# Kernel optimization log

Measured on AMD Instinct MI355X. Metric: run time of the kernel, lower is better.

Reference implementation:

```python
import jax, jax.numpy as jnp
import numpy as np
from jax import lax

# ---- static config (from BasePllay_2 / AdTopoLayer(out_features=50, T=25, m0=0.2, lims=[[224,0],[0,224]], K_max=2, p=0)) ----
H = W = 28
G = H * W
T = 25
K_MAX = 2
M0 = 0.2
OUT_FEATURES = 50
B = 32
TSEQ = jnp.linspace(0.0, 100.0, T)  # fixed landscape sample grid (covers DTM value range)

# static grid geometry from lims=[[224,0],[0,224]]
_xs = np.linspace(224.0, 0.0, H)
_ys = np.linspace(0.0, 224.0, W)
_pts = np.stack(np.meshgrid(_xs, _ys, indexing="ij"), -1).reshape(G, 2)
_d = np.sqrt(((_pts[:, None] - _pts[None]) ** 2).sum(-1))
_sidx = np.argsort(_d, axis=-1)
SDIST = jnp.asarray(np.take_along_axis(_d, _sidx, -1), jnp.float32)  # [G,G] sorted distances per grid point
SIDX = jnp.asarray(_sidx.astype(np.int32))                            # [G,G] static distance-sort order

# 4-connectivity neighbor table for the cubical (pixel) grid, -1 = invalid
_ii = np.arange(G).reshape(H, W)
_nb = np.full((H, W, 4), -1, np.int32)
_nb[1:, :, 0] = _ii[:-1, :]
_nb[:-1, :, 1] = _ii[1:, :]
_nb[:, 1:, 2] = _ii[:, :-1]
_nb[:, :-1, 3] = _ii[:, 1:]
NBR = jnp.asarray(_nb.reshape(G, 4))


def dtm(w):
    """Weighted distance-to-measure (r=2) on the fixed grid. w: [B,G] nonneg -> [B,G]."""
    sw = w[:, SIDX]                               # [B,G,G] weights in distance order
    cw = jnp.cumsum(sw, -1)
    d2 = SDIST ** 2
    cwd = jnp.cumsum(sw * d2[None], -1)
    bound = M0 * w.sum(-1)                        # [B]
    k = jnp.argmax(cw >= bound[:, None, None], -1)  # [B,G] first index reaching mass bound
    km1 = jnp.maximum(k - 1, 0)
    take = lambda a, i: jnp.take_along_axis(a, i[..., None], -1)[..., 0]
    has_prev = k > 0
    cw_p = jnp.where(has_prev, take(cw, km1), 0.0)
    cwd_p = jnp.where(has_prev, take(cwd, km1), 0.0)
    dk2 = d2[jnp.arange(G)[None, :], k]           # [B,G]
    val = (cwd_p + (bound[:, None] - cw_p) * dk2) / bound[:, None]
    return jnp.sqrt(jnp.maximum(val, 0.0))


def pd0(vals):
    """0-dim sublevel-set persistence of vals on the pixel grid (union-find, elder rule).
    Returns (births[G], deaths[G]); non-merging pixels yield zero-persistence pairs,
    essential components die at the max filtration value."""
    order = jnp.argsort(vals).astype(jnp.int32)
    rank = jnp.zeros(G, jnp.int32).at[order].set(jnp.arange(G, dtype=jnp.int32))

    def find(parent, i):
        return lax.while_loop(lambda j: parent[j] != j, lambda j: parent[j], i)

    def step(s, carry):
        parent, death = carry
        p = order[s]
        best = p
        for t in range(4):  # unrolled over the 4 grid neighbors (static)
            q = NBR[p, t]
            ok = (q >= 0) & (rank[jnp.maximum(q, 0)] < s)  # neighbor already inserted
            r = find(parent, jnp.where(ok, q, p))
            merge = ok & (r != best)
            r_old = rank[r] < rank[best]
            older = jnp.where(r_old, r, best)
            younger = jnp.where(r_old, best, r)
            widx = jnp.where(merge, younger, G)   # slot G is a dummy
            parent = parent.at[widx].set(older)
            death = death.at[widx].set(p)         # younger component dies at pixel p
            best = jnp.where(merge, older, best)
        return parent, death

    parent0 = jnp.arange(G + 1, dtype=jnp.int32)
    death0 = jnp.full(G + 1, -1, jnp.int32)
    _, death = lax.fori_loop(0, G, step, (parent0, death0))
    d = death[:G]
    deaths = jnp.where(d >= 0, vals[jnp.maximum(d, 0)], vals.max())
    return vals, deaths


def landscape(births, deaths):
    """K_MAX persistence landscapes sampled at TSEQ. [B,G] -> [B, K_MAX*T]."""
    tb = TSEQ[None, :, None] - births[:, None, :]   # [B,T,G]
    td = deaths[:, None, :] - TSEQ[None, :, None]
    tent = jnp.maximum(jnp.minimum(tb, td), 0.0)
    topk = lax.top_k(tent, K_MAX)[0]                # [B,T,K]
    return jnp.transpose(topk, (0, 2, 1)).reshape(births.shape[0], K_MAX * T)


def _forward(x, w_land, b_land, w_fc, b_fc):
    w = x.reshape(x.shape[0], -1)          # nn.Flatten: pixel intensities as measure weights
    v = dtm(w)                             # [B,G]
    births, deaths = jax.vmap(pd0)(v)
    feats = landscape(births, deaths)      # [B, 50]
    xt = feats @ w_land.T + b_land         # AdTopoLayer output [B, out_features]
    signal = jnp.abs(lax.stop_gradient(xt)).sum(0)   # torch: x.detach().abs().sum(0)
    out = jnp.maximum(xt, 0.0) @ w_fc.T + b_fc       # fc(relu(x))
    return out, signal

_forward_jit = jax.jit(_forward)


def setup_inputs() -> dict:
    key = jax.random.key(0)
    k = jax.random.split(key, 4)
    x = jax.random.uniform(k[0], (B, 1, H, W), jnp.float32)  # image-like nonneg weights
    w_land = jax.random.normal(k[1], (OUT_FEATURES, K_MAX * T), jnp.float32) * 0.1
    b_land = jnp.zeros((OUT_FEATURES,), jnp.float32)
    w_fc = jax.random.normal(k[2], (10, OUT_FEATURES), jnp.float32) * 0.1
    b_fc = jnp.zeros((10,), jnp.float32)
    return {"x": x, "w_land": w_land, "b_land": b_land, "w_fc": w_fc, "b_fc": b_fc}


def reference(x, w_land, b_land, w_fc, b_fc):
    return _forward_jit(x, w_land, b_land, w_fc, b_fc)
```

## Files before the change

### kernel.cpp

```cpp
#include <hip/hip_runtime.h>
#include <math.h>

#define H28 28
#define G784 784
#define BATCH 32
#define NOFF 3025
#define NOFFP 3072
#define NKEY 1459
#define TPTS 25
#define KMAX 2
#define NFEAT 50
#define OUTF 50
#define NCLS 10

#define NBX 16
#define BT 512
#define BT2 512
#define HS 2048
#define EMAX 1024

struct OffPair { unsigned ij; float d2; };
struct OffTab  { OffPair e[NOFFP]; };

constexpr double csqrt(double x) {
  double r = x * 0.5 + 1.0;
  for (int i = 0; i < 20; i++) r = 0.5 * (r + x / r);
  return r;
}

constexpr OffTab make_offtab() {
  OffTab t{};
  int start[NKEY] = {};
  for (int i = 0; i < NOFF; i++) {
    int di = i / 55 - 27, dj = i % 55 - 27;
    start[di * di + dj * dj]++;
  }
  int run = 0;
  for (int k = 0; k < NKEY; k++) { int h = start[k]; start[k] = run; run += h; }
  for (int i = 0; i < NOFF; i++) {
    int di = i / 55 - 27, dj = i % 55 - 27;
    int key = di * di + dj * dj;
    int pos = start[key]++;
    float sd = (key == 0) ? 0.0f : (float)(csqrt((double)key) * (224.0 / 27.0));
    t.e[pos].ij = ((unsigned)(di & 0xffff)) | (((unsigned)(dj & 0xffff)) << 16);
    t.e[pos].d2 = sd * sd;
  }
  for (int i = NOFF; i < NOFFP; i++) { t.e[i].ij = 0x00640064u; t.e[i].d2 = 0.f; }
  return t;
}

__device__ constexpr OffTab OFFTAB = make_offtab();

__device__ __forceinline__ float wave_iscan_f32(float x) {
  int t;
  t = __builtin_amdgcn_update_dpp(0, __float_as_int(x), 0x111, 0xf, 0xf, true);
  x += __int_as_float(t);
  t = __builtin_amdgcn_update_dpp(0, __float_as_int(x), 0x112, 0xf, 0xf, true);
  x += __int_as_float(t);
  t = __builtin_amdgcn_update_dpp(0, __float_as_int(x), 0x114, 0xf, 0xf, true);
  x += __int_as_float(t);
  t = __builtin_amdgcn_update_dpp(0, __float_as_int(x), 0x118, 0xf, 0xf, true);
  x += __int_as_float(t);
  t = __builtin_amdgcn_update_dpp(0, __float_as_int(x), 0x142, 0xa, 0xf, true);
  x += __int_as_float(t);
  t = __builtin_amdgcn_update_dpp(0, __float_as_int(x), 0x143, 0xc, 0xf, true);
  x += __int_as_float(t);
  return x;
}

__global__ __launch_bounds__(BT) void dtm_kernel(const float* __restrict__ x,
                                                 float* __restrict__ v,
                                                 int* __restrict__ done_ctr) {
  __shared__ float w_s[G784];
  __shared__ float red[BT];

  const int tid = threadIdx.x;
  const int b   = blockIdx.x;
  const int bx  = blockIdx.y;

  if (b == 0 && bx == 0 && tid == 0) *done_ctr = 0;

  float ps = 0.f;
  for (int i = tid; i < G784; i += BT) {
    float wv = x[b * G784 + i];
    w_s[i] = wv;
    ps += wv;
  }
  red[tid] = ps;
  __syncthreads();
  for (int off = BT / 2; off > 0; off >>= 1) {
    if (tid < off) red[tid] += red[tid + off];
    __syncthreads();
  }
  const float bound = 0.2f * red[0];

  const int wave = tid >> 6;
  const int lane = tid & 63;
  const int slot = bx * 8 + wave;

  for (int g = slot; g < G784; g += NBX * 8) {
    const int i1 = g / H28, j1 = g % H28;
    float cw = 0.f, cwd = 0.f;
    float cwp = 0.f, cwdp = 0.f, dk2 = 0.f;
    bool crossed = false;
    int o = lane;
    unsigned ij = OFFTAB.e[o].ij;
    float d2v   = OFFTAB.e[o].d2;
    for (int base = 0; base < NOFFP && !crossed; base += 64) {
      int onext = o + 64;
      if (onext >= NOFFP) onext = o;
      const unsigned ij_n = OFFTAB.e[onext].ij;
      const float    d2_n = OFFTAB.e[onext].d2;
      const int di = (short)(ij & 0xffffu);
      const int dj = (short)(ij >> 16);
      const int i2 = i1 + di, j2 = j1 + dj;
      const bool inb = ((unsigned)i2 < (unsigned)H28) & ((unsigned)j2 < (unsigned)H28);
      const float wv = inb ? w_s[i2 * H28 + j2] : 0.f;
      const float wd = wv * d2v;
      const float psw = wave_iscan_f32(wv);
      const float psd = wave_iscan_f32(wd);
      const unsigned long long mask = __ballot(cw + psw >= bound);
      if (mask) {
        const int f = __ffsll((unsigned long long)mask) - 1;
        const float psw_f = __shfl(psw, f);
        const float w_f   = __shfl(wv, f);
        const float psd_f = __shfl(psd, f);
        const float wd_f  = __shfl(wd, f);
        dk2  = __shfl(d2v, f);
        cwp  = cw + (psw_f - w_f);
        cwdp = cwd + (psd_f - wd_f);
        crossed = true;
      } else {
        cw  += __int_as_float(__builtin_amdgcn_readlane(__float_as_int(psw), 63));
        cwd += __int_as_float(__builtin_amdgcn_readlane(__float_as_int(psd), 63));
      }
      ij = ij_n; d2v = d2_n; o = onext;
    }
    const float val = (cwdp + (bound - cwp) * dk2) / bound;
    if (lane == 0) v[b * G784 + g] = sqrtf(fmaxf(val, 0.f));
  }
}

__device__ __forceinline__ unsigned long long pix_key(const float* val_s, int p) {
  return (((unsigned long long)__float_as_uint(val_s[p])) << 10) | (unsigned)p;
}

__global__ __launch_bounds__(BT2) void pd0_kernel(const float* __restrict__ v,
                                                  float* __restrict__ feats,
                                                  int* __restrict__ done_ctr,
                                                  const float* __restrict__ w_land,
                                                  const float* __restrict__ b_land,
                                                  const float* __restrict__ w_fc,
                                                  const float* __restrict__ b_fc,
                                                  float* __restrict__ out) {
  __shared__ float val_s[G784];
  __shared__ int   ptr_s[G784];
  __shared__ int   parent[G784];
  __shared__ unsigned rank_s[G784];
  __shared__ unsigned claims[G784];
  __shared__ float deathv[G784];
  __shared__ int   mlist[G784];
  __shared__ unsigned long long oldkey[G784];
  __shared__ unsigned htag[HS];
  __shared__ unsigned long long hval[HS];
  __shared__ unsigned long long edges[EMAX];
  __shared__ float redf[BT2];
  __shared__ int   mcnt_sh, ecnt_sh, last_sh;
  __shared__ float vmax_sh;
  __shared__ float f_s[BATCH * NFEAT];
  __shared__ float xt_s[BATCH * OUTF];

  const int tid = threadIdx.x;
  const int b   = blockIdx.x;
  if (tid == 0) { mcnt_sh = 0; ecnt_sh = 0; }

  for (int i = tid; i < HS; i += BT2) { htag[i] = 0u; hval[i] = ~0ULL; }

  float pm = -1e30f;
  for (int i = tid; i < G784; i += BT2) {
    float xv = v[b * G784 + i];
    val_s[i] = xv;
    pm = fmaxf(pm, xv);
    rank_s[i] = 0u;
    claims[i] = 0xFFFFFFFFu;
  }
  redf[tid] = pm;
  __syncthreads();
  for (int off = BT2 / 2; off > 0; off >>= 1) {
    if (tid < off) redf[tid] = fmaxf(redf[tid], redf[tid + off]);
    __syncthreads();
  }
  if (tid == 0) vmax_sh = redf[0];
  __syncthreads();
  const float vmax = vmax_sh;

  for (int p = tid; p < G784; p += BT2) {
    unsigned long long kp = pix_key(val_s, p);
    int i = p / H28, j = p % H28;
    int nbs[4];
    nbs[0] = (i > 0)       ? p - H28 : -1;
    nbs[1] = (i < H28 - 1) ? p + H28 : -1;
    nbs[2] = (j > 0)       ? p - 1   : -1;
    nbs[3] = (j < H28 - 1) ? p + 1   : -1;
    int best = p;
    unsigned long long bk = kp;
    for (int t = 0; t < 4; t++) {
      int q = nbs[t];
      if (q >= 0) {
        unsigned long long kq = pix_key(val_s, q);
        if (kq < bk) { bk = kq; best = q; }
      }
    }
    ptr_s[p]  = best;
    parent[p] = p;
    deathv[p] = vmax;
    if (best == p) {
      oldkey[p] = kp;
      int mi = atomicAdd(&mcnt_sh, 1);
      mlist[mi] = p;
    }
  }
  __syncthreads();

  for (int r = 0; r < 10; r++) {
    for (int p = tid; p < G784; p += BT2) ptr_s[p] = ptr_s[ptr_s[p]];
    __syncthreads();
  }

  for (int p = tid; p < G784; p += BT2) {
    unsigned long long kp = pix_key(val_s, p);
    int i = p / H28, j = p % H28;
    int nbs[4];
    nbs[0] = (i > 0)       ? p - H28 : -1;
    nbs[1] = (i < H28 - 1) ? p + H28 : -1;
    nbs[2] = (j > 0)       ? p - 1   : -1;
    nbs[3] = (j < H28 - 1) ? p + 1   : -1;
    int bp = ptr_s[p];
    for (int t = 0; t < 4; t++) {
      int q = nbs[t];
      if (q >= 0) {
        unsigned long long kq = pix_key(val_s, q);
        int bq = ptr_s[q];
        if (kq < kp && bq != bp) {
          unsigned long long key =
              (((unsigned long long)__float_as_uint(val_s[p])) << 32) |
              (((unsigned long long)(unsigned)p) << 22) |
              (((unsigned long long)(unsigned)t) << 20) |
              (((unsigned long long)(unsigned)bp) << 10) |
              ((unsigned long long)(unsigned)bq);
          unsigned lo = (bp < bq) ? (unsigned)bp : (unsigned)bq;
          unsigned hi = (bp < bq) ? (unsigned)bq : (unsigned)bp;
          unsigned pairid = (lo << 10) | hi;
          unsigned idx = (pairid * 2654435761u) >> 21;
          for (;;) {
            unsigned t0 = atomicCAS(&htag[idx], 0u, pairid + 1u);
            if (t0 == 0u || t0 == pairid + 1u) { atomicMin(&hval[idx], key); break; }
            idx = (idx + 1) & (HS - 1);
          }
        }
      }
    }
  }
  __syncthreads();

  for (int i = tid; i < HS; i += BT2) {
    if (htag[i]) {
      int e = atomicAdd(&ecnt_sh, 1);
      if (e < EMAX) edges[e] = hval[i];
    }
  }
  __syncthreads();
  const int ne   = (ecnt_sh < EMAX) ? ecnt_sh : EMAX;
  const int mcnt = mcnt_sh;
  const int wave = tid >> 6;
  const int lane = tid & 63;

  if (wave == 0) {
    if (ne > 1) {
      int n2 = 1;
      while (n2 < ne) n2 <<= 1;
      for (int i = ne + lane; i < n2; i += 64) edges[i] = ~0ULL;
      __threadfence_block();
      for (int kk = 2; kk <= n2; kk <<= 1) {
        for (int jj = kk >> 1; jj > 0; jj >>= 1) {
          for (int i = lane; i < n2; i += 64) {
            int ixj = i ^ jj;
            if (ixj > i) {
              unsigned long long a = edges[i], c = edges[ixj];
              bool up = ((i & kk) == 0);
              if ((a > c) == up) { edges[i] = c; edges[ixj] = a; }
            }
          }
          __threadfence_block();
        }
      }
    }

    int merged = 0;
    const int target = mcnt - 1;
    for (int base = 0; base < ne && merged < target; base += 64) {
      const int idx = base + lane;
      bool unresolved = (idx < ne);
      const unsigned long long e = unresolved ? edges[idx] : 0ULL;
      const int A  = (int)((e >> 10) & 1023u);
      const int Bq = (int)(e & 1023u);
      const float ev = __uint_as_float((unsigned)(e >> 32));
      for (;;) {
        int rA = A, rB = Bq;
        if (unresolved) {
          int xx = A;
          for (;;) { int p1 = parent[xx]; if (p1 == xx) break;
                     int p2 = parent[p1]; parent[xx] = p2; xx = p2; }
          rA = xx;
          xx = Bq;
          for (;;) { int p1 = parent[xx]; if (p1 == xx) break;
                     int p2 = parent[p1]; parent[xx] = p2; xx = p2; }
          rB = xx;
        }
        bool crossing = unresolved && (rA != rB);
        if (unresolved && !crossing) unresolved = false;
        if (__ballot(crossing) == 0ULL) break;
        if (crossing) {
          atomicMin(&claims[rA], (unsigned)lane);
          atomicMin(&claims[rB], (unsigned)lane);
        }
        __threadfence_block();
        bool win = crossing && claims[rA] == (unsigned)lane
                            && claims[rB] == (unsigned)lane;
        __threadfence_block();
        if (crossing) { claims[rA] = 0xFFFFFFFFu; claims[rB] = 0xFFFFFFFFu; }
        if (win) {
          unsigned long long ka = oldkey[rA], kb = oldkey[rB];
          unsigned ra_ = rank_s[rA], rb_ = rank_s[rB];
          int big   = (ra_ > rb_) ? rA : ((rb_ > ra_) ? rB : ((rA < rB) ? rA : rB));
          int small = (big == rA) ? rB : rA;
          parent[small] = big;
          if (ra_ == rb_) rank_s[big] = ra_ + 1u;
          unsigned long long okmin = (ka < kb) ? ka : kb;
          unsigned long long okmax = (ka < kb) ? kb : ka;
          oldkey[big] = okmin;
          int dying = (int)(okmax & 1023u);
          deathv[dying] = ev;
          unresolved = false;
        }
        __threadfence_block();
        merged += (int)__popcll(__ballot(win));
        if (merged >= target) break;
      }
    }
    __threadfence_block();

    if (lane < TPTS) {
      float ti = (float)((double)lane * (100.0 / 24.0));
      float t1 = 0.f, t2 = 0.f;
      for (int ii = 0; ii < mcnt; ii++) {
        int m = mlist[ii];
        float tent = fminf(ti - val_s[m], deathv[m] - ti);
        tent = fmaxf(tent, 0.f);
        if (tent > t1)      { t2 = t1; t1 = tent; }
        else if (tent > t2) { t2 = tent; }
      }
      feats[b * NFEAT + lane]        = t1;
      feats[b * NFEAT + TPTS + lane] = t2;
    }
  }

  __threadfence();
  __syncthreads();
  if (tid == 0) last_sh = (atomicAdd(done_ctr, 1) == BATCH - 1) ? 1 : 0;
  __syncthreads();
  if (!last_sh) return;
  __threadfence();

  for (int i = tid; i < BATCH * NFEAT; i += BT2) f_s[i] = feats[i];
  __syncthreads();
  for (int idx = tid; idx < BATCH * OUTF; idx += BT2) {
    int bb = idx / OUTF, ff = idx % OUTF;
    float acc = b_land[ff];
    const float* wr = w_land + ff * NFEAT;
    const float* fr = f_s + bb * NFEAT;
    for (int j = 0; j < NFEAT; j++) acc += fr[j] * wr[j];
    xt_s[idx] = acc;
  }
  __syncthreads();
  if (tid < OUTF) {
    float s = 0.f;
    for (int bb = 0; bb < BATCH; bb++) s += fabsf(xt_s[bb * OUTF + tid]);
    out[BATCH * NCLS + tid] = s;
  }
  for (int idx = tid; idx < BATCH * NCLS; idx += BT2) {
    int bb = idx / NCLS, cc = idx % NCLS;
    float acc = b_fc[cc];
    const float* wr = w_fc + cc * OUTF;
    const float* xr = xt_s + bb * OUTF;
    for (int ff = 0; ff < OUTF; ff++) acc += fmaxf(xr[ff], 0.f) * wr[ff];
    out[bb * NCLS + cc] = acc;
  }
}

extern "C" void kernel_launch(void* const* d_in, const int* in_sizes, int n_in,
                              void* d_out, int out_size, void* d_ws, size_t ws_size,
                              hipStream_t stream) {
  (void)in_sizes; (void)n_in; (void)out_size; (void)ws_size;
  const float* x      = (const float*)d_in[0];
  const float* w_land = (const float*)d_in[1];
  const float* b_land = (const float*)d_in[2];
  const float* w_fc   = (const float*)d_in[3];
  const float* b_fc   = (const float*)d_in[4];
  float* out   = (float*)d_out;
  float* v     = (float*)d_ws;
  float* feats = v + BATCH * G784;
  int*   done  = (int*)(feats + BATCH * NFEAT);

  dim3 g1(BATCH, NBX);
  dtm_kernel<<<g1, BT, 0, stream>>>(x, v, done);
  pd0_kernel<<<BATCH, BT2, 0, stream>>>(v, feats, done,
                                        w_land, b_land, w_fc, b_fc, out);
}
```

Before: 100.5 us.

## Shrink persistence kernel to one wave, replace bitonic sort with rank sort

```diff
diff --git a/kernel.cpp b/kernel.cpp
--- a/kernel.cpp
+++ b/kernel.cpp
@@ -13,11 +13,12 @@
 #define OUTF 50
 #define NCLS 10
 
-#define NBX 16
+#define NBX 28
 #define BT 512
-#define BT2 512
+#define BT2 64
 #define HS 2048
 #define EMAX 1024
+#define RMAX 16
 
 struct OffPair { unsigned ij; float d2; };
 struct OffTab  { OffPair e[NOFFP]; };
@@ -72,11 +73,13 @@
                                                  float* __restrict__ v,
                                                  int* __restrict__ done_ctr) {
   __shared__ float w_s[G784];
-  __shared__ float red[BT];
-
-  const int tid = threadIdx.x;
-  const int b   = blockIdx.x;
-  const int bx  = blockIdx.y;
+  __shared__ float red[BT / 64];
+
+  const int tid  = threadIdx.x;
+  const int b    = blockIdx.x;
+  const int bx   = blockIdx.y;
+  const int wave = tid >> 6;
+  const int lane = tid & 63;
 
   if (b == 0 && bx == 0 && tid == 0) *done_ctr = 0;
 
@@ -86,16 +89,13 @@
     w_s[i] = wv;
     ps += wv;
   }
-  red[tid] = ps;
-  __syncthreads();
-  for (int off = BT / 2; off > 0; off >>= 1) {
-    if (tid < off) red[tid] += red[tid + off];
-    __syncthreads();
-  }
-  const float bound = 0.2f * red[0];
-
-  const int wave = tid >> 6;
-  const int lane = tid & 63;
+  for (int off = 32; off > 0; off >>= 1) ps += __shfl_xor(ps, off);
+  if (lane == 0) red[wave] = ps;
+  __syncthreads();
+  float tot = 0.f;
+  for (int k = 0; k < BT / 64; k++) tot += red[k];
+  const float bound = 0.2f * tot;
+
   const int slot = bx * 8 + wave;
 
   for (int g = slot; g < G784; g += NBX * 8) {
@@ -164,37 +164,28 @@
   __shared__ unsigned htag[HS];
   __shared__ unsigned long long hval[HS];
   __shared__ unsigned long long edges[EMAX];
-  __shared__ float redf[BT2];
   __shared__ int   mcnt_sh, ecnt_sh, last_sh;
-  __shared__ float vmax_sh;
-  __shared__ float f_s[BATCH * NFEAT];
   __shared__ float xt_s[BATCH * OUTF];
 
-  const int tid = threadIdx.x;
-  const int b   = blockIdx.x;
-  if (tid == 0) { mcnt_sh = 0; ecnt_sh = 0; }
-
-  for (int i = tid; i < HS; i += BT2) { htag[i] = 0u; hval[i] = ~0ULL; }
+  const int lane = threadIdx.x;
+  const int b    = blockIdx.x;
+  if (lane == 0) { mcnt_sh = 0; ecnt_sh = 0; }
+
+  for (int i = lane; i < HS; i += BT2) { htag[i] = 0u; hval[i] = ~0ULL; }
 
   float pm = -1e30f;
-  for (int i = tid; i < G784; i += BT2) {
+  for (int i = lane; i < G784; i += BT2) {
     float xv = v[b * G784 + i];
     val_s[i] = xv;
     pm = fmaxf(pm, xv);
     rank_s[i] = 0u;
     claims[i] = 0xFFFFFFFFu;
   }
-  redf[tid] = pm;
-  __syncthreads();
-  for (int off = BT2 / 2; off > 0; off >>= 1) {
-    if (tid < off) redf[tid] = fmaxf(redf[tid], redf[tid + off]);
-    __syncthreads();
-  }
-  if (tid == 0) vmax_sh = redf[0];
-  __syncthreads();
-  const float vmax = vmax_sh;
-
-  for (int p = tid; p < G784; p += BT2) {
+  for (int off = 32; off > 0; off >>= 1) pm = fmaxf(pm, __shfl_xor(pm, off));
+  const float vmax = pm;
+  __syncthreads();
+
+  for (int p = lane; p < G784; p += BT2) {
     unsigned long long kp = pix_key(val_s, p);
     int i = p / H28, j = p % H28;
     int nbs[4];
@@ -223,11 +214,17 @@
   __syncthreads();
 
   for (int r = 0; r < 10; r++) {
-    for (int p = tid; p < G784; p += BT2) ptr_s[p] = ptr_s[ptr_s[p]];
+    bool ch = false;
+    for (int p = lane; p < G784; p += BT2) {
+      int a = ptr_s[p];
+      int c = ptr_s[a];
+      if (a != c) { ptr_s[p] = c; ch = true; }
+    }
     __syncthreads();
-  }
-
-  for (int p = tid; p < G784; p += BT2) {
+    if (__ballot(ch) == 0ULL) break;
+  }
+
+  for (int p = lane; p < G784; p += BT2) {
     unsigned long long kp = pix_key(val_s, p);
     int i = p / H28, j = p % H28;
     int nbs[4];
@@ -263,7 +260,7 @@
   }
   __syncthreads();
 
-  for (int i = tid; i < HS; i += BT2) {
+  for (int i = lane; i < HS; i += BT2) {
     if (htag[i]) {
       int e = atomicAdd(&ecnt_sh, 1);
       if (e < EMAX) edges[e] = hval[i];
@@ -272,36 +269,26 @@
   __syncthreads();
   const int ne   = (ecnt_sh < EMAX) ? ecnt_sh : EMAX;
   const int mcnt = mcnt_sh;
-  const int wave = tid >> 6;
-  const int lane = tid & 63;
-
-  if (wave == 0) {
-    if (ne > 1) {
-      int n2 = 1;
-      while (n2 < ne) n2 <<= 1;
-      for (int i = ne + lane; i < n2; i += 64) edges[i] = ~0ULL;
-      __threadfence_block();
-      for (int kk = 2; kk <= n2; kk <<= 1) {
-        for (int jj = kk >> 1; jj > 0; jj >>= 1) {
-          for (int i = lane; i < n2; i += 64) {
-            int ixj = i ^ jj;
-            if (ixj > i) {
-              unsigned long long a = edges[i], c = edges[ixj];
-              bool up = ((i & kk) == 0);
-              if ((a > c) == up) { edges[i] = c; edges[ixj] = a; }
-            }
-          }
-          __threadfence_block();
-        }
-      }
-    }
-
+
+  unsigned long long mine[RMAX];
+  int rnk[RMAX];
+  int cnt = 0;
+  for (int i = lane; i < ne; i += BT2) { mine[cnt] = edges[i]; rnk[cnt] = 0; cnt++; }
+  for (int j = 0; j < ne; j++) {
+    unsigned long long ej = edges[j];
+    for (int k = 0; k < cnt; k++) rnk[k] += (ej < mine[k]) ? 1 : 0;
+  }
+  for (int k = 0; k < cnt; k++) hval[rnk[k]] = mine[k];
+  __syncthreads();
+  const unsigned long long* sedges = hval;
+
+  {
     int merged = 0;
     const int target = mcnt - 1;
     for (int base = 0; base < ne && merged < target; base += 64) {
       const int idx = base + lane;
       bool unresolved = (idx < ne);
-      const unsigned long long e = unresolved ? edges[idx] : 0ULL;
+      const unsigned long long e = unresolved ? sedges[idx] : 0ULL;
       const int A  = (int)((e >> 10) & 1023u);
       const int Bq = (int)(e & 1023u);
       const float ev = __uint_as_float((unsigned)(e >> 32));
@@ -324,10 +311,10 @@
           atomicMin(&claims[rA], (unsigned)lane);
           atomicMin(&claims[rB], (unsigned)lane);
         }
-        __threadfence_block();
+        __syncthreads();
         bool win = crossing && claims[rA] == (unsigned)lane
                             && claims[rB] == (unsigned)lane;
-        __threadfence_block();
+        __syncthreads();
         if (crossing) { claims[rA] = 0xFFFFFFFFu; claims[rB] = 0xFFFFFFFFu; }
         if (win) {
           unsigned long long ka = oldkey[rA], kb = oldkey[rB];
@@ -343,52 +330,50 @@
           deathv[dying] = ev;
           unresolved = false;
         }
-        __threadfence_block();
+        __syncthreads();
         merged += (int)__popcll(__ballot(win));
         if (merged >= target) break;
       }
     }
-    __threadfence_block();
-
-    if (lane < TPTS) {
-      float ti = (float)((double)lane * (100.0 / 24.0));
-      float t1 = 0.f, t2 = 0.f;
-      for (int ii = 0; ii < mcnt; ii++) {
-        int m = mlist[ii];
-        float tent = fminf(ti - val_s[m], deathv[m] - ti);
-        tent = fmaxf(tent, 0.f);
-        if (tent > t1)      { t2 = t1; t1 = tent; }
-        else if (tent > t2) { t2 = tent; }
-      }
-      feats[b * NFEAT + lane]        = t1;
-      feats[b * NFEAT + TPTS + lane] = t2;
-    }
+  }
+  __syncthreads();
+
+  if (lane < TPTS) {
+    float ti = (float)((double)lane * (100.0 / 24.0));
+    float t1 = 0.f, t2 = 0.f;
+    for (int ii = 0; ii < mcnt; ii++) {
+      int m = mlist[ii];
+      float tent = fminf(ti - val_s[m], deathv[m] - ti);
+      tent = fmaxf(tent, 0.f);
+      if (tent > t1)      { t2 = t1; t1 = tent; }
+      else if (tent > t2) { t2 = tent; }
+    }
+    feats[b * NFEAT + lane]        = t1;
+    feats[b * NFEAT + TPTS + lane] = t2;
   }
 
   __threadfence();
   __syncthreads();
-  if (tid == 0) last_sh = (atomicAdd(done_ctr, 1) == BATCH - 1) ? 1 : 0;
+  if (lane == 0) last_sh = (atomicAdd(done_ctr, 1) == BATCH - 1) ? 1 : 0;
   __syncthreads();
   if (!last_sh) return;
   __threadfence();
 
-  for (int i = tid; i < BATCH * NFEAT; i += BT2) f_s[i] = feats[i];
-  __syncthreads();
-  for (int idx = tid; idx < BATCH * OUTF; idx += BT2) {
+  for (int idx = lane; idx < BATCH * OUTF; idx += BT2) {
     int bb = idx / OUTF, ff = idx % OUTF;
     float acc = b_land[ff];
     const float* wr = w_land + ff * NFEAT;
-    const float* fr = f_s + bb * NFEAT;
+    const float* fr = feats + bb * NFEAT;
     for (int j = 0; j < NFEAT; j++) acc += fr[j] * wr[j];
     xt_s[idx] = acc;
   }
   __syncthreads();
-  if (tid < OUTF) {
+  if (lane < OUTF) {
     float s = 0.f;
-    for (int bb = 0; bb < BATCH; bb++) s += fabsf(xt_s[bb * OUTF + tid]);
-    out[BATCH * NCLS + tid] = s;
-  }
-  for (int idx = tid; idx < BATCH * NCLS; idx += BT2) {
+    for (int bb = 0; bb < BATCH; bb++) s += fabsf(xt_s[bb * OUTF + lane]);
+    out[BATCH * NCLS + lane] = s;
+  }
+  for (int idx = lane; idx < BATCH * NCLS; idx += BT2) {
     int bb = idx / NCLS, cc = idx % NCLS;
     float acc = b_fc[cc];
     const float* wr = w_fc + cc * OUTF;
```

New measurement: 147.1 us. 1.46x slower.
